# Kernel optimization log

Hardware: AMD Instinct MI355X
Metric: run time of the kernel (lower is better)

The kernel has to match this reference:

```python
import math
import jax, jax.numpy as jnp
import numpy as np

B, T, C, H = 2, 2048, 1024, 16
HD = C // H
ALPHA = 32.0


def setup_inputs() -> dict:
    key = jax.random.key(0)
    ks = jax.random.split(key, 16)
    s = 0.02
    inp = {
        "query": jax.random.normal(ks[0], (B, T, C), jnp.float32),
        "key": jax.random.normal(ks[1], (B, T, C), jnp.float32),
        "value": jax.random.normal(ks[2], (B, T, C), jnp.float32),
        # causal mask: 0 => masked (matches masked_fill(att_mask == 0, -inf))
        "att_mask": jnp.tril(jnp.ones((1, 1, T, T), jnp.float32)),
        "Wq": jax.random.normal(ks[3], (C, C), jnp.float32) * s,
        "bq": jnp.zeros((C,), jnp.float32),
        "Wk": jax.random.normal(ks[4], (C, C), jnp.float32) * s,
        "bk": jnp.zeros((C,), jnp.float32),
        "Wv": jax.random.normal(ks[5], (C, C), jnp.float32) * s,
        "bv": jnp.zeros((C,), jnp.float32),
        "Wp": jax.random.normal(ks[6], (C, C), jnp.float32) * s,
        "bp": jnp.zeros((C,), jnp.float32),
    }
    return inp


def reference(query, key, value, att_mask, Wq, bq, Wk, bk, Wv, bv, Wp, bp):
    b, tq, c = query.shape
    tk = key.shape[1]
    # separate QKV projections, split heads: [B,H,T,HD]
    q = (query @ Wq + bq).reshape(b, tq, H, HD).transpose(0, 2, 1, 3)
    k = (key @ Wk + bk).reshape(b, tk, H, HD).transpose(0, 2, 1, 3)
    v = (value @ Wv + bv).reshape(b, tk, H, HD).transpose(0, 2, 1, 3)
    # PBrelax: pre-scale q by 1/(alpha*sqrt(hd)), subtract detached global abs-max, rescale
    att = jnp.einsum("bhqd,bhkd->bhqk", q * (1.0 / ALPHA / math.sqrt(HD)), k)
    att = (att - jax.lax.stop_gradient(jnp.max(jnp.abs(att)))) * ALPHA
    att = jnp.where(att_mask[:, :, :tq, :tk] == 0, -jnp.inf, att)
    att = jax.nn.softmax(att, axis=-1)
    y = jnp.einsum("bhqk,bhkd->bhqd", att, v)
    y = y.transpose(0, 2, 1, 3).reshape(b, tq, c)
    return y @ Wp + bp
```

## Files before the change

### kernel.cpp

```cpp
#include <hip/hip_runtime.h>


#define Bsz 2
#define Tsz 2048
#define Csz 1024
#define Hsz 16
#define HDsz 64

typedef __bf16 bf16;
typedef __bf16 bf16x8 __attribute__((ext_vector_type(8)));
typedef __bf16 bf16x4 __attribute__((ext_vector_type(4)));
typedef float float4v __attribute__((ext_vector_type(4)));

#define MFMA16(a, b, c) __builtin_amdgcn_mfma_f32_16x16x32_bf16(a, b, c, 0, 0, 0)

#define GLOAD_LDS16(gptr, lptr)                                      \
  __builtin_amdgcn_global_load_lds(                                  \
      (const __attribute__((address_space(1))) void*)(gptr),         \
      (__attribute__((address_space(3))) void*)(lptr), 16, 0, 0)

__global__ __launch_bounds__(256) void cast3_bf16(
    const float* __restrict__ q, const float* __restrict__ k,
    const float* __restrict__ v, bf16* __restrict__ oq,
    bf16* __restrict__ ok, bf16* __restrict__ ov) {
  const int z = blockIdx.z;
  const float* src = z == 0 ? q : (z == 1 ? k : v);
  bf16* dst = z == 0 ? oq : (z == 1 ? ok : ov);
  const size_t i = ((size_t)blockIdx.x * 256 + threadIdx.x) * 8;
  const float4 a = *(const float4*)(src + i);
  const float4 b = *(const float4*)(src + i + 4);
  bf16x8 o;
  o[0] = (bf16)a.x; o[1] = (bf16)a.y; o[2] = (bf16)a.z; o[3] = (bf16)a.w;
  o[4] = (bf16)b.x; o[5] = (bf16)b.y; o[6] = (bf16)b.z; o[7] = (bf16)b.w;
  *(bf16x8*)(dst + i) = o;
}

__global__ __launch_bounds__(256) void wtrans_bf16(
    const float* __restrict__ Wq, const float* __restrict__ Wk,
    const float* __restrict__ Wv, const float* __restrict__ Wp,
    bf16* __restrict__ WT) {
  const int z = blockIdx.z;
  const float* W = z == 0 ? Wq : (z == 1 ? Wk : (z == 2 ? Wv : Wp));
  bf16* out = WT + (size_t)z * (Csz * Csz);
  __shared__ float Ts[64][68];
  const int k0 = blockIdx.y * 64, n0 = blockIdx.x * 64;
  const int tid = threadIdx.x;
#pragma unroll
  for (int it = 0; it < 4; ++it) {
    const int idx = it * 256 + tid;
    const int r = idx >> 4, c4 = (idx & 15) * 4;
    *(float4*)&Ts[r][c4] = *(const float4*)(W + (size_t)(k0 + r) * Csz + n0 + c4);
  }
  __syncthreads();
#pragma unroll
  for (int it = 0; it < 2; ++it) {
    const int idx = it * 256 + tid;
    const int n = idx & 63, k8 = (idx >> 6) * 8;
    bf16x8 o;
#pragma unroll
    for (int j = 0; j < 8; ++j) o[j] = (bf16)Ts[k8 + j][n];
    *(bf16x8*)(out + (size_t)(n0 + n) * Csz + k0 + k8) = o;
  }
}

template <typename OutT, bool VTR>
__global__ __launch_bounds__(256) void gemm_mfma(
    const bf16* __restrict__ A0, const bf16* __restrict__ A1,
    const bf16* __restrict__ A2, const bf16* __restrict__ Wt,
    const float* __restrict__ b0, const float* __restrict__ b1,
    const float* __restrict__ b2, OutT* __restrict__ C0,
    OutT* __restrict__ C1, OutT* __restrict__ C2, int M, int N, int K) {
  const int z = blockIdx.z;
  const bf16* A = z == 0 ? A0 : (z == 1 ? A1 : A2);
  const float* bias = z == 0 ? b0 : (z == 1 ? b1 : b2);
  OutT* C = z == 0 ? C0 : (z == 1 ? C1 : C2);
  const bf16* Bt = Wt + (size_t)z * N * K;
  const float osc = (VTR && z == 0) ? 0.180336880111124f : 1.0f;

  __shared__ bf16 As[128 * 32];
  __shared__ bf16 Bs[128 * 32];
  const int tid = threadIdx.x;
  const int wave = tid >> 6, lane = tid & 63;
  const int l15 = lane & 15, quad = lane >> 4;
  const int m0 = blockIdx.y * 128, n0 = blockIdx.x * 128;
  const int wm = (wave >> 1) * 64, wn = (wave & 1) * 64;
  const int srow = tid >> 2, schunk = tid & 3;

  float4v acc[4][4];
#pragma unroll
  for (int i = 0; i < 4; ++i)
#pragma unroll
    for (int j = 0; j < 4; ++j) acc[i][j] = (float4v){0.f, 0.f, 0.f, 0.f};

  for (int k0 = 0; k0 < K; k0 += 32) {
    __syncthreads();
#pragma unroll
    for (int p = 0; p < 2; ++p) {
      const int row = p * 64 + srow;
      GLOAD_LDS16(A + (size_t)(m0 + row) * K + k0 + schunk * 8,
                  &As[(p * 256 + tid) * 8]);
      GLOAD_LDS16(Bt + (size_t)(n0 + row) * K + k0 + schunk * 8,
                  &Bs[(p * 256 + tid) * 8]);
    }
    __syncthreads();

    bf16x8 af[4], bfr[4];
#pragma unroll
    for (int i = 0; i < 4; ++i)
      af[i] = *(const bf16x8*)&As[(wm + i * 16 + l15) * 32 + quad * 8];
#pragma unroll
    for (int j = 0; j < 4; ++j)
      bfr[j] = *(const bf16x8*)&Bs[(wn + j * 16 + l15) * 32 + quad * 8];
#pragma unroll
    for (int i = 0; i < 4; ++i)
#pragma unroll
      for (int j = 0; j < 4; ++j)
        acc[i][j] = MFMA16(af[i], bfr[j], acc[i][j]);
  }

  const int omb = m0 + wm + quad * 4;
  const int onb = n0 + wn + l15;
  if (VTR && z == 2) {
#pragma unroll
    for (int j = 0; j < 4; ++j) {
      const int n = onb + j * 16;
      const float bj = bias[n];
#pragma unroll
      for (int i = 0; i < 4; ++i) {
        const int mrow = omb + i * 16;
        const int bb = mrow >> 11, t = mrow & (Tsz - 1);
        union { bf16 h[4]; uint2 u; } pk;
#pragma unroll
        for (int r = 0; r < 4; ++r) pk.h[r] = (bf16)(acc[i][j][r] + bj);
        *(uint2*)((bf16*)C + ((size_t)(bb * 1024 + n)) * Tsz + t) = pk.u;
      }
    }
  } else {
#pragma unroll
    for (int j = 0; j < 4; ++j) {
      const float bj = bias[onb + j * 16];
#pragma unroll
      for (int i = 0; i < 4; ++i) {
#pragma unroll
        for (int r = 0; r < 4; ++r) {
          const float v = (acc[i][j][r] + bj) * osc;
          const size_t off = (size_t)(omb + i * 16 + r) * N + onb + j * 16;
          if constexpr (sizeof(OutT) == 2)
            C[off] = (OutT)v;
          else
            C[off] = v;
        }
      }
    }
  }
}

__global__ __launch_bounds__(256) void attn_mfma(const bf16* __restrict__ Q,
                                                 const bf16* __restrict__ K,
                                                 const bf16* __restrict__ Vt,
                                                 bf16* __restrict__ Y) {
  __shared__ bf16 Ks[2][64 * 64];
  __shared__ bf16 Vs[2][64 * 64];
  __shared__ bf16 Ps[4][32 * 72];

  const int bh = blockIdx.y;
  const int b = bh >> 4, h = bh & 15;
  const int i0 = (int)(gridDim.x - 1 - blockIdx.x) * 128;
  const int tid = threadIdx.x;
  const int wave = tid >> 6, lane = tid & 63;
  const int l15 = lane & 15, quad = lane >> 4;

  const int srow = tid >> 3;
  const int sch = tid & 7;

  const bf16* kb = K + (size_t)b * Tsz * Csz + h * HDsz;
  const bf16* vb = Vt + (size_t)bh * HDsz * Tsz;

  const int qb = i0 + wave * 32;

  bf16x8 qf[2][2];
#pragma unroll
  for (int sub = 0; sub < 2; ++sub) {
    const bf16* qp =
        Q + ((size_t)(b * Tsz + qb + sub * 16 + l15)) * Csz + h * HDsz + quad * 8;
    qf[sub][0] = *(const bf16x8*)qp;
    qf[sub][1] = *(const bf16x8*)(qp + 32);
  }

  bf16x8 ones;
#pragma unroll
  for (int j = 0; j < 8; ++j) ones[j] = (bf16)1.0f;

  float4v Of[2][4];
  float4v accl[2];
#pragma unroll
  for (int sub = 0; sub < 2; ++sub) {
    accl[sub] = (float4v){0.f, 0.f, 0.f, 0.f};
#pragma unroll
    for (int nc = 0; nc < 4; ++nc) Of[sub][nc] = (float4v){0.f, 0.f, 0.f, 0.f};
  }

  const int ntile = i0 / 64 + 2;

#pragma unroll
  for (int p = 0; p < 2; ++p) {
    const int r = p * 32 + srow;
    const int c = sch ^ (r & 7);
    GLOAD_LDS16(kb + (size_t)r * Csz + c * 8, &Ks[0][(p * 256 + tid) * 8]);
    GLOAD_LDS16(vb + (size_t)r * Tsz + c * 8, &Vs[0][(p * 256 + tid) * 8]);
  }

  for (int t = 0; t < ntile; ++t) {
    const int j0 = t * 64;
    const int buf = t & 1;
    __syncthreads();
    if (t + 1 < ntile) {
#pragma unroll
      for (int p = 0; p < 2; ++p) {
        const int r = p * 32 + srow;
        const int c = sch ^ (r & 7);
        GLOAD_LDS16(kb + (size_t)(j0 + 64 + r) * Csz + c * 8,
                    &Ks[buf ^ 1][(p * 256 + tid) * 8]);
        GLOAD_LDS16(vb + (size_t)r * Tsz + (j0 + 64) + c * 8,
                    &Vs[buf ^ 1][(p * 256 + tid) * 8]);
      }
    }

    if (j0 <= qb + 31) {
      float4v S[2][4];
#pragma unroll
      for (int nc = 0; nc < 4; ++nc) {
        const int row = nc * 16 + l15;
        const bf16x8 k0 =
            *(const bf16x8*)&Ks[buf][row * 64 + ((quad ^ (row & 7)) * 8)];
        const bf16x8 k1 =
            *(const bf16x8*)&Ks[buf][row * 64 + (((quad + 4) ^ (row & 7)) * 8)];
#pragma unroll
        for (int sub = 0; sub < 2; ++sub) {
          float4v a = (float4v){0.f, 0.f, 0.f, 0.f};
          a = MFMA16(k0, qf[sub][0], a);
          a = MFMA16(k1, qf[sub][1], a);
          S[sub][nc] = a;
        }
      }

      if (j0 + 63 > qb) {
#pragma unroll
        for (int sub = 0; sub < 2; ++sub) {
          const int q = qb + sub * 16 + l15;
#pragma unroll
          for (int nc = 0; nc < 4; ++nc) {
            const int keyb = j0 + nc * 16 + quad * 4;
#pragma unroll
            for (int r = 0; r < 4; ++r)
              if (keyb + r > q) S[sub][nc][r] = -1e30f;
          }
        }
      }

#pragma unroll
      for (int sub = 0; sub < 2; ++sub) {
#pragma unroll
        for (int nc = 0; nc < 4; ++nc) {
          bf16x4 pk;
#pragma unroll
          for (int r = 0; r < 4; ++r)
            pk[r] = (bf16)__builtin_amdgcn_exp2f(S[sub][nc][r]);
          *(bf16x4*)&Ps[wave][(sub * 16 + l15) * 72 + nc * 16 + quad * 4] = pk;
        }
      }

      bf16x8 pf[2][2];
#pragma unroll
      for (int sub = 0; sub < 2; ++sub) {
#pragma unroll
        for (int kc = 0; kc < 2; ++kc)
          pf[sub][kc] = *(const bf16x8*)
              &Ps[wave][(sub * 16 + l15) * 72 + kc * 32 + quad * 8];
        accl[sub] = MFMA16(ones, pf[sub][0], accl[sub]);
        accl[sub] = MFMA16(ones, pf[sub][1], accl[sub]);
      }
#pragma unroll
      for (int nc = 0; nc < 4; ++nc) {
        const int row = nc * 16 + l15;
#pragma unroll
        for (int kc = 0; kc < 2; ++kc) {
          const bf16x8 vf = *(const bf16x8*)
              &Vs[buf][row * 64 + (((kc * 4 + quad) ^ (row & 7)) * 8)];
#pragma unroll
          for (int sub = 0; sub < 2; ++sub)
            Of[sub][nc] = MFMA16(vf, pf[sub][kc], Of[sub][nc]);
        }
      }
    }
  }

#pragma unroll
  for (int sub = 0; sub < 2; ++sub) {
    const float rl = __builtin_amdgcn_rcpf(accl[sub][0]);
    const size_t rowoff =
        ((size_t)(b * Tsz + qb + sub * 16 + l15)) * Csz + h * HDsz;
#pragma unroll
    for (int nc = 0; nc < 4; ++nc) {
      union { bf16 h4[4]; uint2 u; } pk;
#pragma unroll
      for (int r = 0; r < 4; ++r) pk.h4[r] = (bf16)(Of[sub][nc][r] * rl);
      *(uint2*)(Y + rowoff + nc * 16 + quad * 4) = pk.u;
    }
  }
}

extern "C" void kernel_launch(void* const* d_in, const int* in_sizes, int n_in,
                              void* d_out, int out_size, void* d_ws,
                              size_t ws_size, hipStream_t stream) {
  const float* query = (const float*)d_in[0];
  const float* key = (const float*)d_in[1];
  const float* value = (const float*)d_in[2];
  const float* Wq = (const float*)d_in[4];
  const float* bq = (const float*)d_in[5];
  const float* Wk = (const float*)d_in[6];
  const float* bk = (const float*)d_in[7];
  const float* Wv = (const float*)d_in[8];
  const float* bv = (const float*)d_in[9];
  const float* Wp = (const float*)d_in[10];
  const float* bp = (const float*)d_in[11];
  float* out = (float*)d_out;

  char* ws = (char*)d_ws;
  bf16* WT = (bf16*)(ws);
  bf16* vc = (bf16*)(ws + (8u << 20));
  bf16* Qp = (bf16*)(ws + (16u << 20));
  bf16* Kp = (bf16*)(ws + (24u << 20));
  bf16* Vt = (bf16*)(ws + (32u << 20));
  bf16* Yb = vc;
  bf16* qc = (bf16*)d_out;
  bf16* kc = (bf16*)((char*)d_out + (8u << 20));

  const int M = Bsz * Tsz;

  cast3_bf16<<<dim3((M * Csz) / (256 * 8), 1, 3), dim3(256), 0, stream>>>(
      query, key, value, qc, kc, vc);
  wtrans_bf16<<<dim3(16, 16, 4), dim3(256), 0, stream>>>(Wq, Wk, Wv, Wp, WT);
  gemm_mfma<bf16, true><<<dim3(Csz / 128, M / 128, 3), dim3(256), 0, stream>>>(
      qc, kc, vc, WT, bq, bk, bv, Qp, Kp, Vt, M, Csz, Csz);
  attn_mfma<<<dim3(Tsz / 128, Bsz * Hsz), dim3(256), 0, stream>>>(Qp, Kp, Vt,
                                                                  Yb);
  gemm_mfma<float, false><<<dim3(Csz / 128, M / 128, 1), dim3(256), 0, stream>>>(
      Yb, Yb, Yb, WT + 3u * (Csz * Csz), bp, bp, bp, out, out, out, M, Csz,
      Csz);
}
```

Measured before the change: 271.4 us.

## Add 256x256-tile pipelined QKV projection GEMM with 512 threads

Replaces the 128x128 QKV projection GEMM with a new kernel using 256x256 tiles, 8 waves, K-step 64, and double-buffered LDS fed by direct global-to-LDS loads. Reads use an XOR swizzle to avoid bank conflicts. Loads are interleaved with four MFMA phases per k-step, using barriers and setprio to overlap memory with compute. The larger tiles cut global traffic per FLOP, but the grid shrinks to 4x16x3 = 192 blocks, and the Q/K epilogue writes scalar bf16 stores.

```diff
diff --git a/kernel.cpp b/kernel.cpp
--- a/kernel.cpp
+++ b/kernel.cpp
@@ -63,6 +63,193 @@
   }
 }
 
+__global__ __launch_bounds__(512, 2) void gemm256_qkv(
+    const bf16* __restrict__ A0, const bf16* __restrict__ A1,
+    const bf16* __restrict__ A2, const bf16* __restrict__ Wt,
+    const float* __restrict__ b0, const float* __restrict__ b1,
+    const float* __restrict__ b2, bf16* __restrict__ C0,
+    bf16* __restrict__ C1, bf16* __restrict__ Vt) {
+  constexpr int NT = Csz / 64;
+  const int z = blockIdx.z;
+  const bf16* A = z == 0 ? A0 : (z == 1 ? A1 : A2);
+  const float* bias = z == 0 ? b0 : (z == 1 ? b1 : b2);
+  const bf16* Bt = Wt + (size_t)z * (Csz * Csz);
+  const int m0 = blockIdx.y * 256;
+  const int nz0 = blockIdx.x * 256;
+
+  __shared__ bf16 As[2 * 256 * 64];
+  __shared__ bf16 Bs[2 * 256 * 64];
+
+  const int tid = threadIdx.x;
+  const int wave = tid >> 6, lane = tid & 63;
+  const int l15 = lane & 15, quad = lane >> 4;
+  const int wm = wave >> 2, wn = wave & 3;
+
+  const int srow = tid >> 3;
+  const int sch = tid & 7;
+  const bf16* Ab = A + (size_t)(m0 + srow) * Csz + (sch ^ (srow & 7)) * 8;
+  const bf16* Bb = Bt + (size_t)(nz0 + srow) * Csz + (sch ^ (srow & 7)) * 8;
+
+#define STG(Xb, lds, lbuf, hh, tt)                                           \
+  {                                                                          \
+    GLOAD_LDS16((Xb) + (size_t)((hh)*128) * Csz + (size_t)(tt)*64,           \
+                &(lds)[(lbuf) * (256 * 64) + (hh)*8192 + tid * 8]);          \
+    GLOAD_LDS16((Xb) + (size_t)((hh)*128 + 64) * Csz + (size_t)(tt)*64,     \
+                &(lds)[(lbuf) * (256 * 64) + (hh)*8192 + 4096 + tid * 8]);  \
+  }
+#define RD_A(dst, lbuf, i2, ks)                                              \
+  dst = *(const bf16x8*)&As[(lbuf) * (256 * 64) +                            \
+                            (wm * 128 + (i2)*16 + l15) * 64 +                \
+                            ((((ks)*4 + quad) ^ (l15 & 7)) * 8)];
+#define RD_B(dst, lbuf, j2, ks)                                              \
+  dst = *(const bf16x8*)&Bs[(lbuf) * (256 * 64) +                            \
+                            (wn * 64 + (j2)*16 + l15) * 64 +                 \
+                            ((((ks)*4 + quad) ^ (l15 & 7)) * 8)];
+
+  float4v acc[8][4];
+#pragma unroll
+  for (int i = 0; i < 8; ++i)
+#pragma unroll
+    for (int j = 0; j < 4; ++j) acc[i][j] = (float4v){0.f, 0.f, 0.f, 0.f};
+
+  STG(Ab, As, 0, 0, 0);
+  STG(Ab, As, 0, 1, 0);
+  STG(Bb, Bs, 0, 0, 0);
+  STG(Bb, Bs, 0, 1, 0);
+  STG(Ab, As, 1, 0, 1);
+  STG(Ab, As, 1, 1, 1);
+  asm volatile("s_waitcnt vmcnt(4)" ::: "memory");
+  __builtin_amdgcn_s_barrier();
+  __builtin_amdgcn_sched_barrier(0);
+
+#pragma unroll 1
+  for (int t = 0; t < NT; ++t) {
+    const int bsel = t & 1;
+    bf16x8 af0[4][2], af1[4][2], bf0[2][2], bf1[2][2];
+
+#pragma unroll
+    for (int i = 0; i < 4; ++i) {
+      RD_A(af0[i][0], bsel, i, 0);
+      RD_A(af0[i][1], bsel, i, 1);
+    }
+#pragma unroll
+    for (int j = 0; j < 2; ++j) {
+      RD_B(bf0[j][0], bsel, j, 0);
+      RD_B(bf0[j][1], bsel, j, 1);
+    }
+    if (t + 1 < NT) STG(Bb, Bs, bsel ^ 1, 0, t + 1);
+    __builtin_amdgcn_s_barrier();
+    asm volatile("s_waitcnt lgkmcnt(0)" ::: "memory");
+    __builtin_amdgcn_sched_barrier(0);
+    __builtin_amdgcn_s_setprio(1);
+#pragma unroll
+    for (int i = 0; i < 4; ++i)
+#pragma unroll
+      for (int j = 0; j < 2; ++j) {
+        acc[i][j] = MFMA16(af0[i][0], bf0[j][0], acc[i][j]);
+        acc[i][j] = MFMA16(af0[i][1], bf0[j][1], acc[i][j]);
+      }
+    __builtin_amdgcn_s_setprio(0);
+    __builtin_amdgcn_s_barrier();
+
+#pragma unroll
+    for (int i = 0; i < 4; ++i) {
+      RD_A(af1[i][0], bsel, 4 + i, 0);
+      RD_A(af1[i][1], bsel, 4 + i, 1);
+    }
+    if (t + 1 < NT) STG(Bb, Bs, bsel ^ 1, 1, t + 1);
+    __builtin_amdgcn_s_barrier();
+    asm volatile("s_waitcnt lgkmcnt(0)" ::: "memory");
+    __builtin_amdgcn_sched_barrier(0);
+    __builtin_amdgcn_s_setprio(1);
+#pragma unroll
+    for (int i = 0; i < 4; ++i)
+#pragma unroll
+      for (int j = 0; j < 2; ++j) {
+        acc[4 + i][j] = MFMA16(af1[i][0], bf0[j][0], acc[4 + i][j]);
+        acc[4 + i][j] = MFMA16(af1[i][1], bf0[j][1], acc[4 + i][j]);
+      }
+    __builtin_amdgcn_s_setprio(0);
+    __builtin_amdgcn_s_barrier();
+
+#pragma unroll
+    for (int j = 0; j < 2; ++j) {
+      RD_B(bf1[j][0], bsel, 2 + j, 0);
+      RD_B(bf1[j][1], bsel, 2 + j, 1);
+    }
+    if (t + 2 < NT) STG(Ab, As, bsel, 0, t + 2);
+    __builtin_amdgcn_s_barrier();
+    asm volatile("s_waitcnt lgkmcnt(0)" ::: "memory");
+    __builtin_amdgcn_sched_barrier(0);
+    __builtin_amdgcn_s_setprio(1);
+#pragma unroll
+    for (int i = 0; i < 4; ++i)
+#pragma unroll
+      for (int j = 0; j < 2; ++j) {
+        acc[i][2 + j] = MFMA16(af0[i][0], bf1[j][0], acc[i][2 + j]);
+        acc[i][2 + j] = MFMA16(af0[i][1], bf1[j][1], acc[i][2 + j]);
+      }
+    __builtin_amdgcn_s_setprio(0);
+    __builtin_amdgcn_s_barrier();
+
+    if (t + 2 < NT) STG(Ab, As, bsel, 1, t + 2);
+    __builtin_amdgcn_s_barrier();
+    __builtin_amdgcn_s_setprio(1);
+#pragma unroll
+    for (int i = 0; i < 4; ++i)
+#pragma unroll
+      for (int j = 0; j < 2; ++j) {
+        acc[4 + i][2 + j] = MFMA16(af1[i][0], bf1[j][0], acc[4 + i][2 + j]);
+        acc[4 + i][2 + j] = MFMA16(af1[i][1], bf1[j][1], acc[4 + i][2 + j]);
+      }
+    __builtin_amdgcn_s_setprio(0);
+    if (t + 2 < NT) {
+      asm volatile("s_waitcnt vmcnt(4)" ::: "memory");
+    } else if (t + 1 < NT) {
+      asm volatile("s_waitcnt vmcnt(0)" ::: "memory");
+    }
+    __builtin_amdgcn_s_barrier();
+    __builtin_amdgcn_sched_barrier(0);
+  }
+#undef STG
+#undef RD_A
+#undef RD_B
+
+  const int omb0 = m0 + wm * 128 + quad * 4;
+  const int onb0 = nz0 + wn * 64 + l15;
+  if (z == 2) {
+#pragma unroll
+    for (int j = 0; j < 4; ++j) {
+      const int n = onb0 + j * 16;
+      const float bj = bias[n];
+#pragma unroll
+      for (int i = 0; i < 8; ++i) {
+        const int mrow = omb0 + i * 16;
+        const int bb = mrow >> 11, tt = mrow & (Tsz - 1);
+        union { bf16 h[4]; uint2 u; } pk;
+#pragma unroll
+        for (int r = 0; r < 4; ++r) pk.h[r] = (bf16)(acc[i][j][r] + bj);
+        *(uint2*)(Vt + ((size_t)(bb * 1024 + n)) * Tsz + tt) = pk.u;
+      }
+    }
+  } else {
+    bf16* C = z == 0 ? C0 : C1;
+    const float osc = z == 0 ? 0.180336880111124f : 1.0f;
+#pragma unroll
+    for (int j = 0; j < 4; ++j) {
+      const float bj = bias[onb0 + j * 16];
+#pragma unroll
+      for (int i = 0; i < 8; ++i) {
+#pragma unroll
+        for (int r = 0; r < 4; ++r) {
+          const float v = (acc[i][j][r] + bj) * osc;
+          C[(size_t)(omb0 + i * 16 + r) * Csz + onb0 + j * 16] = (bf16)v;
+        }
+      }
+    }
+  }
+}
+
 template <typename OutT, bool VTR>
 __global__ __launch_bounds__(256) void gemm_mfma(
     const bf16* __restrict__ A0, const bf16* __restrict__ A1,
@@ -341,8 +528,8 @@
   cast3_bf16<<<dim3((M * Csz) / (256 * 8), 1, 3), dim3(256), 0, stream>>>(
       query, key, value, qc, kc, vc);
   wtrans_bf16<<<dim3(16, 16, 4), dim3(256), 0, stream>>>(Wq, Wk, Wv, Wp, WT);
-  gemm_mfma<bf16, true><<<dim3(Csz / 128, M / 128, 3), dim3(256), 0, stream>>>(
-      qc, kc, vc, WT, bq, bk, bv, Qp, Kp, Vt, M, Csz, Csz);
+  gemm256_qkv<<<dim3(Csz / 256, M / 256, 3), dim3(512), 0, stream>>>(
+      qc, kc, vc, WT, bq, bk, bv, Qp, Kp, Vt);
   attn_mfma<<<dim3(Tsz / 128, Bsz * Hsz), dim3(256), 0, stream>>>(Qp, Kp, Vt,
                                                                   Yb);
   gemm_mfma<float, false><<<dim3(Csz / 128, M / 128, 1), dim3(256), 0, stream>>>(
```

New measurement: 257.0 us. 5.3% less time.
